# Kernel tuning notes

Measured on AMD Instinct MI355X. Metric: run time of the kernel, lower is better.

Reference implementation:

```python
import jax, jax.numpy as jnp
import numpy as np
from jax import lax

NEG = -1e30  # finite stand-in for -inf (stable under logaddexp and grads)
B, T, C, L = 256, 512, 256, 128  # batch, time, num_classes (blank = C-1), max label len


def setup_inputs() -> dict:
    key = jax.random.key(0)
    k1, k2, k3 = jax.random.split(key, 3)
    logits = jax.random.normal(k1, (B, T, C), dtype=jnp.float32)
    y_pred = jax.nn.softmax(logits, axis=-1)            # keras expects softmax probs
    y_true = jax.random.randint(k2, (B, L), 0, C - 1).astype(jnp.int32)  # exclude blank
    input_length = jnp.full((B, 1), T, dtype=jnp.int32)
    label_length = jax.random.randint(k3, (B, 1), L // 2, L + 1).astype(jnp.int32)
    return {"y_true": y_true, "y_pred": y_pred,
            "input_length": input_length, "label_length": label_length}


def _ctc_batch_cost(y_true, y_pred, input_length, label_length):
    Bb, Tt, Cc = y_pred.shape
    Ll = y_true.shape[1]
    S = 2 * Ll + 1
    blank = Cc - 1
    # keras ctc_batch_cost: logits = log(y_pred + eps); tf.nn.ctc_loss then applies
    # log_softmax internally (softmax(log p) == p for normalized p, up to eps).
    logp = jax.nn.log_softmax(jnp.log(y_pred + 1e-7), axis=-1)        # [B,T,C]

    # extended label sequence: blank, l1, blank, l2, ..., blank  -> [B,S]
    ext = jnp.full((Bb, S), blank, dtype=jnp.int32)
    ext = ext.at[:, 1::2].set(y_true.astype(jnp.int32))
    same_prev = jnp.concatenate(
        [jnp.ones((Bb, 2), bool), ext[:, 2:] == ext[:, :-2]], axis=1)
    can_skip = (ext != blank) & (~same_prev)                           # [B,S]

    # emission log-prob per extended position: emit[b,t,s] = logp[b,t,ext[b,s]]
    emit = jnp.take_along_axis(
        logp, jnp.broadcast_to(ext[:, None, :], (Bb, Tt, S)), axis=2)  # [B,T,S]

    alpha0 = jnp.full((Bb, S), NEG, dtype=logp.dtype)
    alpha0 = alpha0.at[:, 0].set(emit[:, 0, 0]).at[:, 1].set(emit[:, 0, 1])
    inlen = input_length[:, 0]

    def step(alpha, xs):
        emit_t, t = xs                                    # [B,S], scalar
        s1 = jnp.concatenate([jnp.full((Bb, 1), NEG, alpha.dtype), alpha[:, :-1]], 1)
        s2 = jnp.concatenate([jnp.full((Bb, 2), NEG, alpha.dtype), alpha[:, :-2]], 1)
        s2 = jnp.where(can_skip, s2, NEG)
        new = jnp.logaddexp(jnp.logaddexp(alpha, s1), s2) + emit_t
        alpha = jnp.where((t < inlen)[:, None], new, alpha)  # freeze past input_length
        return alpha, None

    xs = (emit[:, 1:].transpose(1, 0, 2), jnp.arange(1, Tt))
    alphaT, _ = lax.scan(step, alpha0, xs)

    lab = jnp.clip(label_length[:, 0], 1, Ll)
    idx = jnp.stack([2 * lab - 1, 2 * lab], axis=1)                    # [B,2]
    ends = jnp.take_along_axis(alphaT, idx, axis=1)
    loss = -jnp.logaddexp(ends[:, 0], ends[:, 1])                      # [B]
    return loss[:, None]                                               # [B,1] like keras


def reference(y_true, y_pred, input_length, label_length):
    return _ctc_batch_cost(y_true, y_pred, input_length, label_length)
```

## Files before the change

kernel.cpp:

```cpp
#include <hip/hip_runtime.h>
#include <math.h>

#define NEGVF (-1e30f)
#define CTC_T 512
#define CTC_C 256
#define CTC_L 128
#define BLANKC (CTC_C - 1)

#if __has_builtin(__builtin_amdgcn_exp2f)
__device__ __forceinline__ float fexp2(float x) { return __builtin_amdgcn_exp2f(x); }
#else
__device__ __forceinline__ float fexp2(float x) { return exp2f(x); }
#endif
#if __has_builtin(__builtin_amdgcn_logf)
__device__ __forceinline__ float flog2(float x) { return __builtin_amdgcn_logf(x); }
#else
__device__ __forceinline__ float flog2(float x) { return log2f(x); }
#endif

__device__ __forceinline__ float lae2(float a, float b) {
    float m = fmaxf(a, b);
    float n = fminf(a, b);
    return m + flog2(1.0f + fexp2(n - m));
}

__device__ __forceinline__ float dpp_shr1_f(float x) {
    return __int_as_float(__builtin_amdgcn_update_dpp(
        0, __float_as_int(x), 0x138, 0xF, 0xF, true));
}
__device__ __forceinline__ int dpp_shr1_i(int x) {
    return __builtin_amdgcn_update_dpp(0, x, 0x138, 0xF, 0xF, true);
}

__global__ __launch_bounds__(256) void ctc_fwd_kernel(
    const int* __restrict__ y_true,
    const float* __restrict__ y_pred,
    const int* __restrict__ in_len,
    const int* __restrict__ lab_len,
    float* __restrict__ out)
{
    __shared__ float ring[4][8][3][64];
    __shared__ float sh[2 * CTC_L + 1];

    const int b   = blockIdx.x;
    const int tid = threadIdx.x;
    const int wid = tid >> 6;
    const int k   = tid & 63;

    const float* __restrict__ ybase = y_pred + (size_t)b * CTC_T * CTC_C;
    const uint64_t ybase_u = (uint64_t)(uintptr_t)ybase;
    const int* __restrict__ yt = y_true + (size_t)b * CTC_L;

    const int l0 = yt[2 * k];
    const int l1 = yt[2 * k + 1];
    const int lm1 = __shfl_up(l1, 1);
    const float sk1f = ((k > 0) && (l0 != lm1) && (l0 != BLANKC)) ? 1.0f : 0.0f;
    const float sk3f = ((l1 != l0) && (l1 != BLANKC)) ? 1.0f : 0.0f;

    int inl = in_len[b];
    if (inl > CTC_T) inl = CTC_T;
    const int nsteps = inl - 1;
    const int nb2 = (nsteps > 0) ? ((nsteps + 7) >> 3) : 0;

    float pb0 = ybase[BLANKC];
    float p00 = ybase[l0];
    float a0 = (k == 0) ? pb0 : 0.0f;
    float a1 = (k == 0) ? p00 : 0.0f;
    float a2 = 0.0f, a3 = 0.0f, a4 = 0.0f;
    int   E  = 0;
    float pm3raw = 0.0f;

    int v_ofb = BLANKC * 4;
    int v_of0 = l0 * 4;
    int v_of1 = l1 * 4;

#define LOAD1(dst, voff, rb) \
    asm volatile("global_load_dword %0, %1, %2" \
                 : "=v"(dst) : "v"(voff), "s"(rb) : "memory")

    if (nb2 >= 1) {
        if (wid == 0) {
            float pbC = 0, p0C = 0, p1C = 0, pbM = 0, p0M = 0, p1M = 0;
            float pbN = 0, p0N = 0, p1N = 0;

#define RD(rp_, rr, A, Bv, Cv) { \
    A  = (rp_)[(rr) * 192 + k]; \
    Bv = (rp_)[(rr) * 192 + 64 + k]; \
    Cv = (rp_)[(rr) * 192 + 128 + k]; }

#define CARITH(dX) { \
    float pmu = ldexpf(pm3raw, dX); \
    float a3n = fmaf(sk3f, a1, a3 + a2) * p1C; \
    pm3raw = dpp_shr1_f(a3n); \
    float a0n = (a0 + pmu) * pbC; \
    float a1n = fmaf(sk1f, pmu, a1 + a0) * p0C; \
    float a2n = (a2 + a1) * pbC; \
    a4 = (a4 + a3) * pbC; \
    a0 = a0n; a1 = a1n; a2 = a2n; a3 = a3n; }

#define ROT2 { pbC = pbM; p0C = p0M; p1C = p1M; pbM = pbN; p0M = p0N; p1M = p1N; }
#define ROT1 { pbC = pbM; p0C = p0M; p1C = p1M; }

            for (int jj = 0; jj < nb2 + 3; ++jj) {
                __builtin_amdgcn_s_barrier();
                int cj = jj - 3;
                if (cj < 0) continue;
                int tbase = 1 + 8 * cj;
                int rem = nsteps - tbase;
                const float* rp = (const float*)&ring[cj & 3][0][0][0];
                if (cj == 0) {
                    RD(rp, 0, pbC, p0C, p1C);
                    RD(rp, 1, pbM, p0M, p1M);
                }
                int EnbOld = dpp_shr1_i(E);
                float m = fmaxf(fmaxf(fmaxf(a0, a1), fmaxf(a2, a3)), a4);
                float mm = m * 0x1p64f;
                int exm = (__float_as_int(mm) >> 23) & 0xff;
                bool dead = (exm == 0);
                int dd = dead ? 0 : (191 - exm);
                a0 = ldexpf(a0, dd); a1 = ldexpf(a1, dd); a2 = ldexpf(a2, dd);
                a3 = ldexpf(a3, dd); a4 = ldexpf(a4, dd);
                E -= dd;
                int E0 = __builtin_amdgcn_readfirstlane(E);
                E = dead ? E0 : E;
                int Enb = dpp_shr1_i(E);
                int dnb  = Enb - E;
                int dadj = EnbOld - E;
                { RD(rp, 2, pbN, p0N, p1N); CARITH(dadj); ROT2 }
                if (rem > 0) { RD(rp, 3, pbN, p0N, p1N); CARITH(dnb); ROT2 }
                if (rem > 1) { RD(rp, 4, pbN, p0N, p1N); CARITH(dnb); ROT2 }
                if (rem > 2) { RD(rp, 5, pbN, p0N, p1N); CARITH(dnb); ROT2 }
                if (rem > 3) { RD(rp, 6, pbN, p0N, p1N); CARITH(dnb); ROT2 }
                if (rem > 4) { RD(rp, 7, pbN, p0N, p1N); CARITH(dnb); ROT2 }
                if (rem > 5) { CARITH(dnb); ROT1 }
                if (rem > 6) { CARITH(dnb); }
                if (cj + 1 < nb2) {
                    const float* np = (const float*)&ring[(cj + 1) & 3][0][0][0];
                    RD(np, 0, pbC, p0C, p1C);
                    RD(np, 1, pbM, p0M, p1M);
                }
            }
#undef RD
#undef CARITH
#undef ROT2
#undef ROT1
        } else {
            const int p = wid - 1;
            float gpb[8], gp0[8], gp1[8];

#define PROW(r_, t0_) { \
    int rr = (t0_) + (r_); if (rr > nsteps) rr = nsteps; \
    uint64_t rb = ybase_u + (uint64_t)rr * (CTC_C * 4); \
    LOAD1(gpb[r_], v_ofb, rb); \
    LOAD1(gp0[r_], v_of0, rb); \
    LOAD1(gp1[r_], v_of1, rb); }

#define PISSUE(bj_) { \
    int t0 = 1 + 8 * (bj_); \
    PROW(0, t0) PROW(1, t0) PROW(2, t0) PROW(3, t0) \
    PROW(4, t0) PROW(5, t0) PROW(6, t0) PROW(7, t0) }

#define WROW(wp_, r_) { \
    (wp_)[(r_) * 192 + k]        = gpb[r_]; \
    (wp_)[(r_) * 192 + 64 + k]   = gp0[r_]; \
    (wp_)[(r_) * 192 + 128 + k]  = gp1[r_]; }

#define PCOMPLETE(bc_) { \
    asm volatile("s_waitcnt vmcnt(0)" ::: "memory"); \
    __builtin_amdgcn_sched_barrier(0); \
    float* wp = (float*)&ring[(bc_) & 3][0][0][0]; \
    WROW(wp, 0) WROW(wp, 1) WROW(wp, 2) WROW(wp, 3) \
    WROW(wp, 4) WROW(wp, 5) WROW(wp, 6) WROW(wp, 7) \
    asm volatile("s_waitcnt lgkmcnt(0)" ::: "memory"); }

            for (int jj = 0; jj < nb2 + 3; ++jj) {
                __builtin_amdgcn_s_barrier();
                int bc = jj - 1;
                if (bc >= 0 && bc < nb2 && (bc % 3) == p) PCOMPLETE(bc);
                if (jj == 0 && p == 0) PISSUE(0);
                int bi = jj + 1;
                if (bi < nb2 && (bi % 3) == p) PISSUE(bi);
            }
#undef PROW
#undef PISSUE
#undef WROW
#undef PCOMPLETE
        }
    }

    float l0v = fmaxf(flog2(a0) + (float)E, NEGVF);
    float l1v = fmaxf(flog2(a1) + (float)E, NEGVF);
    float l2v = fmaxf(flog2(a2) + (float)E, NEGVF);
    float l3v = fmaxf(flog2(a3) + (float)E, NEGVF);
    float l4v = fmaxf(flog2(a4) + (float)E, NEGVF);

    if (wid == 0) {
        sh[4 * k + 0] = l0v;
        sh[4 * k + 1] = l1v;
        sh[4 * k + 2] = l2v;
        sh[4 * k + 3] = l3v;
        if (k == 63) sh[256] = l4v;
    }
    __syncthreads();
    if (tid == 0) {
        int ll = lab_len[b];
        if (ll < 1) ll = 1;
        if (ll > CTC_L) ll = CTC_L;
        float ea = sh[2 * ll - 1];
        float eb = sh[2 * ll];
        int cnt = 1 + (nsteps > 0 ? nsteps : 0);
        const float LSE2 = flog2(1.0f + (float)CTC_C * 1e-7f);
        out[b] = -0.69314718055994530942f * (lae2(ea, eb) - (float)cnt * LSE2);
    }
#undef LOAD1
}

extern "C" void kernel_launch(void* const* d_in, const int* in_sizes, int n_in,
                              void* d_out, int out_size, void* d_ws, size_t ws_size,
                              hipStream_t stream) {
    (void)n_in; (void)d_ws; (void)ws_size; (void)out_size;
    const int* y_true = (const int*)d_in[0];
    const float* y_pred = (const float*)d_in[1];
    const int* in_len = (const int*)d_in[2];
    const int* lab_len = (const int*)d_in[3];
    float* out = (float*)d_out;
    const int B = in_sizes[2];
    ctc_fwd_kernel<<<B, 256, 0, stream>>>(y_true, y_pred, in_len, lab_len, out);
}
```

Baseline: 38.84 us.

## Stage full probability rows via dwordx4 loads with single producer wave

```diff
diff --git a/kernel.cpp b/kernel.cpp
--- a/kernel.cpp
+++ b/kernel.cpp
@@ -6,6 +6,8 @@
 #define CTC_C 256
 #define CTC_L 128
 #define BLANKC (CTC_C - 1)
+
+typedef float f4 __attribute__((ext_vector_type(4)));
 
 #if __has_builtin(__builtin_amdgcn_exp2f)
 __device__ __forceinline__ float fexp2(float x) { return __builtin_amdgcn_exp2f(x); }
@@ -32,14 +34,14 @@
     return __builtin_amdgcn_update_dpp(0, x, 0x138, 0xF, 0xF, true);
 }
 
-__global__ __launch_bounds__(256) void ctc_fwd_kernel(
+__global__ __launch_bounds__(128) void ctc_fwd_kernel(
     const int* __restrict__ y_true,
     const float* __restrict__ y_pred,
     const int* __restrict__ in_len,
     const int* __restrict__ lab_len,
     float* __restrict__ out)
 {
-    __shared__ float ring[4][8][3][64];
+    __shared__ float ring[4][8][CTC_C];
     __shared__ float sh[2 * CTC_L + 1];
 
     const int b   = blockIdx.x;
@@ -70,23 +72,22 @@
     int   E  = 0;
     float pm3raw = 0.0f;
 
-    int v_ofb = BLANKC * 4;
-    int v_of0 = l0 * 4;
-    int v_of1 = l1 * 4;
-
-#define LOAD1(dst, voff, rb) \
-    asm volatile("global_load_dword %0, %1, %2" \
-                 : "=v"(dst) : "v"(voff), "s"(rb) : "memory")
+    const int v_off4 = k << 4;
+
+#define LOADR(dst, rb) \
+    asm volatile("global_load_dwordx4 %0, %1, %2" \
+                 : "=v"(dst) : "v"(v_off4), "s"(rb) : "memory")
 
     if (nb2 >= 1) {
         if (wid == 0) {
             float pbC = 0, p0C = 0, p1C = 0, pbM = 0, p0M = 0, p1M = 0;
             float pbN = 0, p0N = 0, p1N = 0;
 
-#define RD(rp_, rr, A, Bv, Cv) { \
-    A  = (rp_)[(rr) * 192 + k]; \
-    Bv = (rp_)[(rr) * 192 + 64 + k]; \
-    Cv = (rp_)[(rr) * 192 + 128 + k]; }
+#define RD(S_, r_, A, Bv, Cv) { \
+    const float* rp_ = &ring[S_][r_][0]; \
+    A  = rp_[BLANKC]; \
+    Bv = rp_[l0]; \
+    Cv = rp_[l1]; }
 
 #define CARITH(dX) { \
     float pmu = ldexpf(pm3raw, dX); \
@@ -101,90 +102,106 @@
 #define ROT2 { pbC = pbM; p0C = p0M; p1C = p1M; pbM = pbN; p0M = p0N; p1M = p1N; }
 #define ROT1 { pbC = pbM; p0C = p0M; p1C = p1M; }
 
-            for (int jj = 0; jj < nb2 + 3; ++jj) {
+            for (int jj = 0; jj < nb2 + 2; ++jj) {
+                int cj = jj - 2;
+                if (cj >= 0) {
+                    int tbase = 1 + 8 * cj;
+                    int rem = nsteps - tbase;
+                    int S = cj & 3;
+                    int EnbOld = dpp_shr1_i(E);
+                    float m = fmaxf(fmaxf(fmaxf(a0, a1), fmaxf(a2, a3)), a4);
+                    float mm = m * 0x1p64f;
+                    int exm = (__float_as_int(mm) >> 23) & 0xff;
+                    bool dead = (exm == 0);
+                    int dd = dead ? 0 : (191 - exm);
+                    a0 = ldexpf(a0, dd); a1 = ldexpf(a1, dd); a2 = ldexpf(a2, dd);
+                    a3 = ldexpf(a3, dd); a4 = ldexpf(a4, dd);
+                    E -= dd;
+                    int E0 = __builtin_amdgcn_readfirstlane(E);
+                    E = dead ? E0 : E;
+                    int Enb = dpp_shr1_i(E);
+                    int dnb  = Enb - E;
+                    int dadj = EnbOld - E;
+                    { RD(S, 2, pbN, p0N, p1N); CARITH(dadj); ROT2 }
+                    if (rem > 0) { RD(S, 3, pbN, p0N, p1N); CARITH(dnb); ROT2 }
+                    if (rem > 1) { RD(S, 4, pbN, p0N, p1N); CARITH(dnb); ROT2 }
+                    if (rem > 2) { RD(S, 5, pbN, p0N, p1N); CARITH(dnb); ROT2 }
+                    if (rem > 3) { RD(S, 6, pbN, p0N, p1N); CARITH(dnb); ROT2 }
+                    if (rem > 4) { RD(S, 7, pbN, p0N, p1N); CARITH(dnb); ROT2 }
+                    if (rem > 5) { CARITH(dnb); ROT1 }
+                    if (rem > 6) { CARITH(dnb); }
+                }
+                int nj = jj - 1;
+                if (nj >= 0 && nj < nb2) {
+                    int S2 = nj & 3;
+                    RD(S2, 0, pbC, p0C, p1C);
+                    RD(S2, 1, pbM, p0M, p1M);
+                }
                 __builtin_amdgcn_s_barrier();
-                int cj = jj - 3;
-                if (cj < 0) continue;
-                int tbase = 1 + 8 * cj;
-                int rem = nsteps - tbase;
-                const float* rp = (const float*)&ring[cj & 3][0][0][0];
-                if (cj == 0) {
-                    RD(rp, 0, pbC, p0C, p1C);
-                    RD(rp, 1, pbM, p0M, p1M);
-                }
-                int EnbOld = dpp_shr1_i(E);
-                float m = fmaxf(fmaxf(fmaxf(a0, a1), fmaxf(a2, a3)), a4);
-                float mm = m * 0x1p64f;
-                int exm = (__float_as_int(mm) >> 23) & 0xff;
-                bool dead = (exm == 0);
-                int dd = dead ? 0 : (191 - exm);
-                a0 = ldexpf(a0, dd); a1 = ldexpf(a1, dd); a2 = ldexpf(a2, dd);
-                a3 = ldexpf(a3, dd); a4 = ldexpf(a4, dd);
-                E -= dd;
-                int E0 = __builtin_amdgcn_readfirstlane(E);
-                E = dead ? E0 : E;
-                int Enb = dpp_shr1_i(E);
-                int dnb  = Enb - E;
-                int dadj = EnbOld - E;
-                { RD(rp, 2, pbN, p0N, p1N); CARITH(dadj); ROT2 }
-                if (rem > 0) { RD(rp, 3, pbN, p0N, p1N); CARITH(dnb); ROT2 }
-                if (rem > 1) { RD(rp, 4, pbN, p0N, p1N); CARITH(dnb); ROT2 }
-                if (rem > 2) { RD(rp, 5, pbN, p0N, p1N); CARITH(dnb); ROT2 }
-                if (rem > 3) { RD(rp, 6, pbN, p0N, p1N); CARITH(dnb); ROT2 }
-                if (rem > 4) { RD(rp, 7, pbN, p0N, p1N); CARITH(dnb); ROT2 }
-                if (rem > 5) { CARITH(dnb); ROT1 }
-                if (rem > 6) { CARITH(dnb); }
-                if (cj + 1 < nb2) {
-                    const float* np = (const float*)&ring[(cj + 1) & 3][0][0][0];
-                    RD(np, 0, pbC, p0C, p1C);
-                    RD(np, 1, pbM, p0M, p1M);
-                }
+                asm volatile("" ::: "memory");
             }
 #undef RD
 #undef CARITH
 #undef ROT2
 #undef ROT1
         } else {
-            const int p = wid - 1;
-            float gpb[8], gp0[8], gp1[8];
-
-#define PROW(r_, t0_) { \
-    int rr = (t0_) + (r_); if (rr > nsteps) rr = nsteps; \
-    uint64_t rb = ybase_u + (uint64_t)rr * (CTC_C * 4); \
-    LOAD1(gpb[r_], v_ofb, rb); \
-    LOAD1(gp0[r_], v_of0, rb); \
-    LOAD1(gp1[r_], v_of1, rb); }
-
-#define PISSUE(bj_) { \
-    int t0 = 1 + 8 * (bj_); \
-    PROW(0, t0) PROW(1, t0) PROW(2, t0) PROW(3, t0) \
-    PROW(4, t0) PROW(5, t0) PROW(6, t0) PROW(7, t0) }
-
-#define WROW(wp_, r_) { \
-    (wp_)[(r_) * 192 + k]        = gpb[r_]; \
-    (wp_)[(r_) * 192 + 64 + k]   = gp0[r_]; \
-    (wp_)[(r_) * 192 + 128 + k]  = gp1[r_]; }
-
-#define PCOMPLETE(bc_) { \
-    asm volatile("s_waitcnt vmcnt(0)" ::: "memory"); \
-    __builtin_amdgcn_sched_barrier(0); \
-    float* wp = (float*)&ring[(bc_) & 3][0][0][0]; \
-    WROW(wp, 0) WROW(wp, 1) WROW(wp, 2) WROW(wp, 3) \
-    WROW(wp, 4) WROW(wp, 5) WROW(wp, 6) WROW(wp, 7) \
-    asm volatile("s_waitcnt lgkmcnt(0)" ::: "memory"); }
-
-            for (int jj = 0; jj < nb2 + 3; ++jj) {
-                __builtin_amdgcn_s_barrier();
-                int bc = jj - 1;
-                if (bc >= 0 && bc < nb2 && (bc % 3) == p) PCOMPLETE(bc);
-                if (jj == 0 && p == 0) PISSUE(0);
-                int bi = jj + 1;
-                if (bi < nb2 && (bi % 3) == p) PISSUE(bi);
+            f4 bufA[8], bufB[8];
+
+#define PISSUE(buf, bi_) { \
+    int t0 = 1 + 8 * (bi_); \
+    { int rr = t0 + 0; if (rr > nsteps) rr = nsteps; \
+      uint64_t rb = ybase_u + (uint64_t)rr * 1024; LOADR(buf[0], rb); } \
+    { int rr = t0 + 1; if (rr > nsteps) rr = nsteps; \
+      uint64_t rb = ybase_u + (uint64_t)rr * 1024; LOADR(buf[1], rb); } \
+    { int rr = t0 + 2; if (rr > nsteps) rr = nsteps; \
+      uint64_t rb = ybase_u + (uint64_t)rr * 1024; LOADR(buf[2], rb); } \
+    { int rr = t0 + 3; if (rr > nsteps) rr = nsteps; \
+      uint64_t rb = ybase_u + (uint64_t)rr * 1024; LOADR(buf[3], rb); } \
+    { int rr = t0 + 4; if (rr > nsteps) rr = nsteps; \
+      uint64_t rb = ybase_u + (uint64_t)rr * 1024; LOADR(buf[4], rb); } \
+    { int rr = t0 + 5; if (rr > nsteps) rr = nsteps; \
+      uint64_t rb = ybase_u + (uint64_t)rr * 1024; LOADR(buf[5], rb); } \
+    { int rr = t0 + 6; if (rr > nsteps) rr = nsteps; \
+      uint64_t rb = ybase_u + (uint64_t)rr * 1024; LOADR(buf[6], rb); } \
+    { int rr = t0 + 7; if (rr > nsteps) rr = nsteps; \
+      uint64_t rb = ybase_u + (uint64_t)rr * 1024; LOADR(buf[7], rb); } }
+
+#define PWRITE(buf, S_) { \
+    ((f4*)&ring[S_][0][0])[k] = buf[0]; \
+    ((f4*)&ring[S_][1][0])[k] = buf[1]; \
+    ((f4*)&ring[S_][2][0])[k] = buf[2]; \
+    ((f4*)&ring[S_][3][0])[k] = buf[3]; \
+    ((f4*)&ring[S_][4][0])[k] = buf[4]; \
+    ((f4*)&ring[S_][5][0])[k] = buf[5]; \
+    ((f4*)&ring[S_][6][0])[k] = buf[6]; \
+    ((f4*)&ring[S_][7][0])[k] = buf[7]; }
+
+#define PPERIOD(cur, nxt) { \
+    bool iss = (jj + 1 < nb2); \
+    if (iss) { PISSUE(nxt, jj + 1); } \
+    if (jj < nb2) { \
+        if (iss) { asm volatile("s_waitcnt vmcnt(8)" ::: "memory"); } \
+        else     { asm volatile("s_waitcnt vmcnt(0)" ::: "memory"); } \
+        __builtin_amdgcn_sched_barrier(0); \
+        int S = jj & 3; \
+        PWRITE(cur, S); \
+        asm volatile("s_waitcnt lgkmcnt(0)" ::: "memory"); \
+    } \
+    __builtin_amdgcn_s_barrier(); \
+    ++jj; }
+
+            int jj = 0;
+            __builtin_amdgcn_sched_barrier(0);
+            PISSUE(bufA, 0);
+            for (;;) {
+                PPERIOD(bufA, bufB);
+                if (jj >= nb2 + 2) break;
+                PPERIOD(bufB, bufA);
+                if (jj >= nb2 + 2) break;
             }
-#undef PROW
 #undef PISSUE
-#undef WROW
-#undef PCOMPLETE
+#undef PWRITE
+#undef PPERIOD
         }
     }
 
@@ -212,7 +229,7 @@
         const float LSE2 = flog2(1.0f + (float)CTC_C * 1e-7f);
         out[b] = -0.69314718055994530942f * (lae2(ea, eb) - (float)cnt * LSE2);
     }
-#undef LOAD1
+#undef LOADR
 }
 
 extern "C" void kernel_launch(void* const* d_in, const int* in_sizes, int n_in,
@@ -225,5 +242,5 @@
     const int* lab_len = (const int*)d_in[3];
     float* out = (float*)d_out;
     const int B = in_sizes[2];
-    ctc_fwd_kernel<<<B, 256, 0, stream>>>(y_true, y_pred, in_len, lab_len, out);
-}
+    ctc_fwd_kernel<<<B, 128, 0, stream>>>(y_true, y_pred, in_len, lab_len, out);
+}
```

New measurement: 40.15 us. 3.4% more time.

## Load full probability rows with coalesced dwordx4 and gather labels via LDS scratch

Applied to the files above, without the earlier changes.

```diff
diff --git a/kernel.cpp b/kernel.cpp
--- a/kernel.cpp
+++ b/kernel.cpp
@@ -6,6 +6,9 @@
 #define CTC_C 256
 #define CTC_L 128
 #define BLANKC (CTC_C - 1)
+#define RS 4
+
+typedef float f4 __attribute__((ext_vector_type(4)));
 
 #if __has_builtin(__builtin_amdgcn_exp2f)
 __device__ __forceinline__ float fexp2(float x) { return __builtin_amdgcn_exp2f(x); }
@@ -39,7 +42,8 @@
     const int* __restrict__ lab_len,
     float* __restrict__ out)
 {
-    __shared__ float ring[4][8][3][64];
+    __shared__ float ring[RS][8][3][64];
+    __shared__ float scratch[3][8][CTC_C];
     __shared__ float sh[2 * CTC_L + 1];
 
     const int b   = blockIdx.x;
@@ -70,23 +74,21 @@
     int   E  = 0;
     float pm3raw = 0.0f;
 
-    int v_ofb = BLANKC * 4;
-    int v_of0 = l0 * 4;
-    int v_of1 = l1 * 4;
-
-#define LOAD1(dst, voff, rb) \
-    asm volatile("global_load_dword %0, %1, %2" \
-                 : "=v"(dst) : "v"(voff), "s"(rb) : "memory")
+    const int v_off4 = k << 4;
+
+#define LOADR(dst, rb) \
+    asm volatile("global_load_dwordx4 %0, %1, %2" \
+                 : "=v"(dst) : "v"(v_off4), "s"(rb) : "memory")
 
     if (nb2 >= 1) {
+        const int nper = nb2 + 2;
         if (wid == 0) {
-            float pbC = 0, p0C = 0, p1C = 0, pbM = 0, p0M = 0, p1M = 0;
-            float pbN = 0, p0N = 0, p1N = 0;
-
-#define RD(rp_, rr, A, Bv, Cv) { \
-    A  = (rp_)[(rr) * 192 + k]; \
-    Bv = (rp_)[(rr) * 192 + 64 + k]; \
-    Cv = (rp_)[(rr) * 192 + 128 + k]; }
+            float pbC, p0C, p1C, pbM, p0M, p1M, pbN, p0N, p1N;
+
+#define RDX(rp_, r_, A, Bv, Cv) { \
+    A  = (rp_)[(r_) * 192 + k]; \
+    Bv = (rp_)[(r_) * 192 + 64 + k]; \
+    Cv = (rp_)[(r_) * 192 + 128 + k]; }
 
 #define CARITH(dX) { \
     float pmu = ldexpf(pm3raw, dX); \
@@ -101,90 +103,90 @@
 #define ROT2 { pbC = pbM; p0C = p0M; p1C = p1M; pbM = pbN; p0M = p0N; p1M = p1N; }
 #define ROT1 { pbC = pbM; p0C = p0M; p1C = p1M; }
 
-            for (int jj = 0; jj < nb2 + 3; ++jj) {
+            for (int pp = 0; pp < nper; ++pp) {
+                int cb = pp - 2;
+                if (cb >= 0) {
+                    int tbase = 1 + 8 * cb;
+                    int rem = nsteps - tbase;
+                    const float* rp = &ring[cb & (RS - 1)][0][0][0];
+                    int EnbOld = dpp_shr1_i(E);
+                    float m = fmaxf(fmaxf(fmaxf(a0, a1), fmaxf(a2, a3)), a4);
+                    float mm = m * 0x1p64f;
+                    int exm = (__float_as_int(mm) >> 23) & 0xff;
+                    bool dead = (exm == 0);
+                    int dd = dead ? 0 : (191 - exm);
+                    a0 = ldexpf(a0, dd); a1 = ldexpf(a1, dd); a2 = ldexpf(a2, dd);
+                    a3 = ldexpf(a3, dd); a4 = ldexpf(a4, dd);
+                    E -= dd;
+                    int E0 = __builtin_amdgcn_readfirstlane(E);
+                    E = dead ? E0 : E;
+                    int Enb = dpp_shr1_i(E);
+                    int dnb  = Enb - E;
+                    int dadj = EnbOld - E;
+                    RDX(rp, 0, pbC, p0C, p1C);
+                    RDX(rp, 1, pbM, p0M, p1M);
+                    { RDX(rp, 2, pbN, p0N, p1N); CARITH(dadj); ROT2 }
+                    if (rem > 0) { RDX(rp, 3, pbN, p0N, p1N); CARITH(dnb); ROT2 }
+                    if (rem > 1) { RDX(rp, 4, pbN, p0N, p1N); CARITH(dnb); ROT2 }
+                    if (rem > 2) { RDX(rp, 5, pbN, p0N, p1N); CARITH(dnb); ROT2 }
+                    if (rem > 3) { RDX(rp, 6, pbN, p0N, p1N); CARITH(dnb); ROT2 }
+                    if (rem > 4) { RDX(rp, 7, pbN, p0N, p1N); CARITH(dnb); ROT2 }
+                    if (rem > 5) { CARITH(dnb); ROT1 }
+                    if (rem > 6) { CARITH(dnb); }
+                }
+                asm volatile("s_waitcnt lgkmcnt(0)" ::: "memory");
                 __builtin_amdgcn_s_barrier();
-                int cj = jj - 3;
-                if (cj < 0) continue;
-                int tbase = 1 + 8 * cj;
-                int rem = nsteps - tbase;
-                const float* rp = (const float*)&ring[cj & 3][0][0][0];
-                if (cj == 0) {
-                    RD(rp, 0, pbC, p0C, p1C);
-                    RD(rp, 1, pbM, p0M, p1M);
-                }
-                int EnbOld = dpp_shr1_i(E);
-                float m = fmaxf(fmaxf(fmaxf(a0, a1), fmaxf(a2, a3)), a4);
-                float mm = m * 0x1p64f;
-                int exm = (__float_as_int(mm) >> 23) & 0xff;
-                bool dead = (exm == 0);
-                int dd = dead ? 0 : (191 - exm);
-                a0 = ldexpf(a0, dd); a1 = ldexpf(a1, dd); a2 = ldexpf(a2, dd);
-                a3 = ldexpf(a3, dd); a4 = ldexpf(a4, dd);
-                E -= dd;
-                int E0 = __builtin_amdgcn_readfirstlane(E);
-                E = dead ? E0 : E;
-                int Enb = dpp_shr1_i(E);
-                int dnb  = Enb - E;
-                int dadj = EnbOld - E;
-                { RD(rp, 2, pbN, p0N, p1N); CARITH(dadj); ROT2 }
-                if (rem > 0) { RD(rp, 3, pbN, p0N, p1N); CARITH(dnb); ROT2 }
-                if (rem > 1) { RD(rp, 4, pbN, p0N, p1N); CARITH(dnb); ROT2 }
-                if (rem > 2) { RD(rp, 5, pbN, p0N, p1N); CARITH(dnb); ROT2 }
-                if (rem > 3) { RD(rp, 6, pbN, p0N, p1N); CARITH(dnb); ROT2 }
-                if (rem > 4) { RD(rp, 7, pbN, p0N, p1N); CARITH(dnb); ROT2 }
-                if (rem > 5) { CARITH(dnb); ROT1 }
-                if (rem > 6) { CARITH(dnb); }
-                if (cj + 1 < nb2) {
-                    const float* np = (const float*)&ring[(cj + 1) & 3][0][0][0];
-                    RD(np, 0, pbC, p0C, p1C);
-                    RD(np, 1, pbM, p0M, p1M);
-                }
+                asm volatile("" ::: "memory");
             }
-#undef RD
+#undef RDX
 #undef CARITH
 #undef ROT2
 #undef ROT1
         } else {
             const int p = wid - 1;
-            float gpb[8], gp0[8], gp1[8];
-
-#define PROW(r_, t0_) { \
+            f4 rbuf0, rbuf1, rbuf2, rbuf3, rbuf4, rbuf5, rbuf6, rbuf7;
+
+#define PISS1(dst, r_, t0_) { \
     int rr = (t0_) + (r_); if (rr > nsteps) rr = nsteps; \
-    uint64_t rb = ybase_u + (uint64_t)rr * (CTC_C * 4); \
-    LOAD1(gpb[r_], v_ofb, rb); \
-    LOAD1(gp0[r_], v_of0, rb); \
-    LOAD1(gp1[r_], v_of1, rb); }
-
-#define PISSUE(bj_) { \
-    int t0 = 1 + 8 * (bj_); \
-    PROW(0, t0) PROW(1, t0) PROW(2, t0) PROW(3, t0) \
-    PROW(4, t0) PROW(5, t0) PROW(6, t0) PROW(7, t0) }
-
-#define WROW(wp_, r_) { \
-    (wp_)[(r_) * 192 + k]        = gpb[r_]; \
-    (wp_)[(r_) * 192 + 64 + k]   = gp0[r_]; \
-    (wp_)[(r_) * 192 + 128 + k]  = gp1[r_]; }
-
-#define PCOMPLETE(bc_) { \
-    asm volatile("s_waitcnt vmcnt(0)" ::: "memory"); \
-    __builtin_amdgcn_sched_barrier(0); \
-    float* wp = (float*)&ring[(bc_) & 3][0][0][0]; \
-    WROW(wp, 0) WROW(wp, 1) WROW(wp, 2) WROW(wp, 3) \
-    WROW(wp, 4) WROW(wp, 5) WROW(wp, 6) WROW(wp, 7) \
-    asm volatile("s_waitcnt lgkmcnt(0)" ::: "memory"); }
-
-            for (int jj = 0; jj < nb2 + 3; ++jj) {
+    uint64_t rb = ybase_u + (uint64_t)rr * 1024; \
+    LOADR(dst, rb); }
+
+#define PGATH(dst_r, src) { \
+    ((f4*)&scratch[p][dst_r][0])[k] = (src); }
+
+#define PCOMPACT(S_, r_) { \
+    float pbv = scratch[p][r_][BLANKC]; \
+    float p0v = scratch[p][r_][l0]; \
+    float p1v = scratch[p][r_][l1]; \
+    ring[S_][r_][0][k] = pbv; \
+    ring[S_][r_][1][k] = p0v; \
+    ring[S_][r_][2][k] = p1v; }
+
+            for (int pp = 0; pp < nper; ++pp) {
+                if (pp < nb2 && (pp % 3) == p) {
+                    int t0 = 1 + 8 * pp;
+                    PISS1(rbuf0, 0, t0) PISS1(rbuf1, 1, t0)
+                    PISS1(rbuf2, 2, t0) PISS1(rbuf3, 3, t0)
+                    PISS1(rbuf4, 4, t0) PISS1(rbuf5, 5, t0)
+                    PISS1(rbuf6, 6, t0) PISS1(rbuf7, 7, t0)
+                }
+                int bg = pp - 1;
+                if (bg >= 0 && bg < nb2 && (bg % 3) == p) {
+                    asm volatile("s_waitcnt vmcnt(0)" ::: "memory");
+                    __builtin_amdgcn_sched_barrier(0);
+                    PGATH(0, rbuf0) PGATH(1, rbuf1) PGATH(2, rbuf2) PGATH(3, rbuf3)
+                    PGATH(4, rbuf4) PGATH(5, rbuf5) PGATH(6, rbuf6) PGATH(7, rbuf7)
+                    int S = bg & (RS - 1);
+                    PCOMPACT(S, 0) PCOMPACT(S, 1) PCOMPACT(S, 2) PCOMPACT(S, 3)
+                    PCOMPACT(S, 4) PCOMPACT(S, 5) PCOMPACT(S, 6) PCOMPACT(S, 7)
+                }
+                asm volatile("s_waitcnt lgkmcnt(0)" ::: "memory");
                 __builtin_amdgcn_s_barrier();
-                int bc = jj - 1;
-                if (bc >= 0 && bc < nb2 && (bc % 3) == p) PCOMPLETE(bc);
-                if (jj == 0 && p == 0) PISSUE(0);
-                int bi = jj + 1;
-                if (bi < nb2 && (bi % 3) == p) PISSUE(bi);
+                asm volatile("" ::: "memory");
             }
-#undef PROW
-#undef PISSUE
-#undef WROW
-#undef PCOMPLETE
+#undef PISS1
+#undef PGATH
+#undef PCOMPACT
         }
     }
 
@@ -212,7 +214,7 @@
         const float LSE2 = flog2(1.0f + (float)CTC_C * 1e-7f);
         out[b] = -0.69314718055994530942f * (lae2(ea, eb) - (float)cnt * LSE2);
     }
-#undef LOAD1
+#undef LOADR
 }
 
 extern "C" void kernel_launch(void* const* d_in, const int* in_sizes, int n_in,
```

New measurement: 37.10 us. 4.5% less time.
